# Kernel optimization log

Hardware: AMD Instinct MI355X
Metric: run time of the kernel (lower is better)

Reference implementation:

```python
import jax, jax.numpy as jnp
import numpy as np

SEQ_LEN = 168; PRED_LEN = 24; N_FEAT = 8; KERNEL = 25
N_QUBITS = 4; N_QLAYERS = 2; CONTEXT = 32; HIDDEN = 8; BATCH = 16384
LAG_POSITIONS = [1, 2, 3, 4, 5, 6, 23, 24, 25, 167, 168]
LAG_IDX = np.array([SEQ_LEN - l for l in LAG_POSITIONS if l <= SEQ_LEN])
N_LAGS = int(LAG_IDX.size)
PI = float(np.pi)


def _apply_1q(state, U, w):
    # apply 2x2 gate U (shared (2,2) or per-sample (B,2,2)) on wire w
    state = jnp.moveaxis(state, 1 + w, -1)
    if U.ndim == 2:
        state = jnp.einsum('ij,b...j->b...i', U, state)
    else:
        state = jnp.einsum('bij,b...j->b...i', U, state)
    return jnp.moveaxis(state, -1, 1 + w)


def _apply_cnot(state, c, t):
    ax_c, ax_t = 1 + c, 1 + t
    s0 = jax.lax.index_in_dim(state, 0, ax_c, keepdims=False)
    s1 = jax.lax.index_in_dim(state, 1, ax_c, keepdims=False)
    s1 = jnp.flip(s1, axis=ax_t - (1 if t > c else 0))
    return jnp.stack([s0, s1], axis=ax_c)


def _ry(theta):  # (B,) -> (B,2,2)
    c, s = jnp.cos(theta / 2), jnp.sin(theta / 2)
    return jnp.stack([jnp.stack([c, -s], -1), jnp.stack([s, c], -1)], -2).astype(jnp.complex64)


def _rot(w):  # w (3,): Rot(phi,theta,omega) = RZ(omega) RY(theta) RZ(phi)
    phi, theta, omega = w[0], w[1], w[2]
    c, s = jnp.cos(theta / 2), jnp.sin(theta / 2)
    ep = jnp.exp(-0.5j * (phi + omega))
    em = jnp.exp(0.5j * (phi - omega))
    return jnp.stack([jnp.stack([ep * c, -em * s]),
                      jnp.stack([jnp.conj(em) * s, jnp.conj(ep) * c])]).astype(jnp.complex64)


def _vqc(inputs, weights):
    # data re-uploading: [RY AngleEmbedding -> Rot per wire -> CNOT ring (range 1)] x N_QLAYERS
    # (StronglyEntanglingLayers is called with 1 layer per upload, so range is always 1)
    B = inputs.shape[0]
    state = jnp.zeros((B,) + (2,) * N_QUBITS, jnp.complex64)
    state = state.at[(slice(None),) + (0,) * N_QUBITS].set(1.0)
    for l in range(N_QLAYERS):
        for q in range(N_QUBITS):
            state = _apply_1q(state, _ry(inputs[:, q]), q)
        for q in range(N_QUBITS):
            state = _apply_1q(state, _rot(weights[l, q]), q)
        for q in range(N_QUBITS):
            state = _apply_cnot(state, q, (q + 1) % N_QUBITS)
    probs = state.real ** 2 + state.imag ** 2  # (B,2,2,2,2)
    zdiag = jnp.array([1.0, -1.0], jnp.float32)
    exps = []
    for q in range(N_QUBITS):
        other = tuple(a for a in range(1, N_QUBITS + 1) if a != 1 + q)
        exps.append(jnp.einsum('bq,q->b', probs.sum(other), zdiag))
    return jnp.stack(exps, axis=-1)  # (B, N_QUBITS)


def _decomp(x, decomp_w):
    # learnable moving-average decomposition (DLinear-style, per-feature softmax kernel, edge padding)
    pad = (KERNEL - 1) // 2
    w = jax.nn.softmax(decomp_w, axis=-1)  # (F,K)
    xp = jnp.pad(x, ((0, 0), (pad, KERNEL - 1 - pad), (0, 0)), mode='edge')
    xc = jnp.moveaxis(xp, 1, 2)  # (B,F,S+K-1)
    trend = jax.lax.conv_general_dilated(xc, w[:, None, :], (1,), 'VALID',
                                         feature_group_count=N_FEAT,
                                         dimension_numbers=('NCH', 'OIH', 'NCH'))
    trend = jnp.moveaxis(trend, 1, 2)  # (B,S,F)
    return x - trend, trend


def forward(x, decomp_w, trend_w, trend_b, seasonal_w, seasonal_b, h0_w, h0_b,
            ta_w, ta_b, sc_w, sc_b, crz_w, crz_b, cn_w, cn_b,
            vqc_r, vqc_u, vqc_c, expand_w, expand_b, mod_w, mod_b, fusion_alpha):
    seasonal, trend = _decomp(x, decomp_w)
    trend_out = jnp.einsum('bsf,ps->bpf', trend, trend_w) + trend_b[None, :, None]
    seasonal_base = jnp.einsum('bsf,ps->bpf', seasonal, seasonal_w) + seasonal_b[None, :, None]
    lag_vals = x[:, LAG_IDX, -1]  # (B, N_LAGS), demand is last feature
    h0 = jnp.tanh(lag_vals @ h0_w.T + h0_b)  # (B,H)
    ctx = jnp.einsum('bsf,cs->bfc', seasonal, ta_w) + ta_b  # (B,F,C)
    gru_in = jnp.tanh(ctx.reshape(x.shape[0], -1) @ sc_w.T + sc_b)  # (B,H)
    # single-step quantum GRU
    xh = jnp.concatenate([gru_in, h0], axis=1)  # (B,2H)
    rz_in = jnp.tanh(xh @ crz_w.T + crz_b) * PI  # r_in == z_in (same compress in source)
    r = jax.nn.sigmoid(_vqc(rz_in, vqc_r) @ expand_w.T + expand_b)
    z = jax.nn.sigmoid(_vqc(rz_in, vqc_u) @ expand_w.T + expand_b)
    n_in = jnp.tanh(jnp.concatenate([r * h0, gru_in], axis=1) @ cn_w.T + cn_b) * PI
    n = jnp.tanh(_vqc(n_in, vqc_c) @ expand_w.T + expand_b)
    h_new = (1 - z) * n + z * h0
    modulation = jnp.tanh(h_new @ mod_w.T + mod_b)  # (B,P)
    seasonal_out = seasonal_base * (1.0 + modulation[:, :, None])
    alpha = jax.nn.sigmoid(fusion_alpha)[0]
    return alpha * seasonal_out + (1 - alpha) * trend_out  # (B,P,F)


def setup_inputs() -> dict:
    key = jax.random.key(0)
    ks = iter(jax.random.split(key, 32))

    def lin(out_d, in_d):
        lim = 1.0 / np.sqrt(in_d)
        return (jax.random.uniform(next(ks), (out_d, in_d), jnp.float32, -lim, lim),
                jax.random.uniform(next(ks), (out_d,), jnp.float32, -lim, lim))

    trend_w, trend_b = lin(PRED_LEN, SEQ_LEN)
    seasonal_w, seasonal_b = lin(PRED_LEN, SEQ_LEN)
    h0_w, h0_b = lin(HIDDEN, N_LAGS)
    ta_w, ta_b = lin(CONTEXT, SEQ_LEN)
    sc_w, sc_b = lin(HIDDEN, N_FEAT * CONTEXT)
    crz_w, crz_b = lin(N_QUBITS, 2 * HIDDEN)
    cn_w, cn_b = lin(N_QUBITS, 2 * HIDDEN)
    expand_w, expand_b = lin(HIDDEN, N_QUBITS)
    mod_w, mod_b = lin(PRED_LEN, HIDDEN)
    return {
        'x': jax.random.normal(next(ks), (BATCH, SEQ_LEN, N_FEAT), jnp.float32),
        'decomp_w': 0.02 * jax.random.normal(next(ks), (N_FEAT, KERNEL), jnp.float32),
        'trend_w': trend_w, 'trend_b': trend_b,
        'seasonal_w': seasonal_w, 'seasonal_b': seasonal_b,
        'h0_w': h0_w, 'h0_b': h0_b,
        'ta_w': ta_w, 'ta_b': ta_b,
        'sc_w': sc_w, 'sc_b': sc_b,
        'crz_w': crz_w, 'crz_b': crz_b,
        'cn_w': cn_w, 'cn_b': cn_b,
        'vqc_r': jax.random.uniform(next(ks), (N_QLAYERS, N_QUBITS, 3), jnp.float32, 0.0, 2 * PI),
        'vqc_u': jax.random.uniform(next(ks), (N_QLAYERS, N_QUBITS, 3), jnp.float32, 0.0, 2 * PI),
        'vqc_c': jax.random.uniform(next(ks), (N_QLAYERS, N_QUBITS, 3), jnp.float32, 0.0, 2 * PI),
        'expand_w': expand_w, 'expand_b': expand_b,
        'mod_w': mod_w, 'mod_b': mod_b,
        'fusion_alpha': jnp.array([0.5], jnp.float32),
    }


def reference(x, decomp_w, trend_w, trend_b, seasonal_w, seasonal_b, h0_w, h0_b,
              ta_w, ta_b, sc_w, sc_b, crz_w, crz_b, cn_w, cn_b,
              vqc_r, vqc_u, vqc_c, expand_w, expand_b, mod_w, mod_b, fusion_alpha):
    return forward(x, decomp_w, trend_w, trend_b, seasonal_w, seasonal_b, h0_w, h0_b,
                   ta_w, ta_b, sc_w, sc_b, crz_w, crz_b, cn_w, cn_b,
                   vqc_r, vqc_u, vqc_c, expand_w, expand_b, mod_w, mod_b, fusion_alpha)
```

## Files before the change

kernel.cpp:

```cpp
#include <hip/hip_runtime.h>
#include <hip/hip_bf16.h>
#include <cmath>

#define SEQ   168
#define NF    8
#define PRED  24
#define HID   8
#define KTOT  1344
#define NSCH  6
#define PI_F  3.14159265358979323846f

#define WS_ROTC     256
#define WS_CGIN     512
#define WS_WT       1024
#define WS_IMG_BYTE 524288

typedef __attribute__((ext_vector_type(8))) short bf16x8;
typedef __attribute__((ext_vector_type(4))) float f32x4;

__device__ __forceinline__ float frcp(float x)  { return __builtin_amdgcn_rcpf(x); }
__device__ __forceinline__ float ftanh(float x) {
    float xc = fminf(fmaxf(x, -15.f), 15.f);
    float e  = __expf(2.f * xc);
    return (e - 1.f) * frcp(e + 1.f);
}
__device__ __forceinline__ float sigm(float x) { return frcp(1.f + __expf(-x)); }
__device__ __forceinline__ unsigned short f2bf(float f) {
    __hip_bfloat16 h = __float2bfloat16(f);
    return __builtin_bit_cast(unsigned short, h);
}
__device__ __forceinline__ unsigned pack2(float a, float b) {
    return (unsigned)f2bf(a) | ((unsigned)f2bf(b) << 16);
}

__global__ void k_compose(const float* __restrict__ decomp_w,
                          const float* __restrict__ trend_w,
                          const float* __restrict__ seasonal_w,
                          const float* __restrict__ ta_w,
                          float* __restrict__ Wt) {
    __shared__ float dwsh[NF * 25];
    int t = threadIdx.x;
    if (t < NF) {
        const float* row = decomp_w + t * 25;
        float m = row[0];
        for (int k = 1; k < 25; ++k) m = fmaxf(m, row[k]);
        float e[25]; float sum = 0.f;
        for (int k = 0; k < 25; ++k) { e[k] = expf(row[k] - m); sum += e[k]; }
        float inv = 1.f / sum;
        for (int k = 0; k < 25; ++k) dwsh[t * 25 + k] = e[k] * inv;
    }
    __syncthreads();
    int n = blockIdx.x * 256 + t;
    if (n >= SEQ * 640) return;
    int sx  = n / 640;
    int col = n % 640;
    int j = col >> 3;
    int f = col & 7;
    const float* dwf = dwsh + f * 25;
    const float* wsel;
    int isTrend = 0;
    if (j < 24)      { wsel = trend_w    + j        * SEQ; isTrend = 1; }
    else if (j < 48) { wsel = seasonal_w + (j - 24) * SEQ; }
    else             { wsel = ta_w       + (j - 48) * SEQ; }
    float acc = 0.f;
    if (sx == 0) {
        for (int s = 0; s <= 12; ++s) {
            float cw = 0.f;
            for (int k = 0; k <= 12 - s; ++k) cw += dwf[k];
            acc = fmaf(cw, wsel[s], acc);
        }
    } else if (sx == 167) {
        for (int s = 155; s < 168; ++s) {
            float cw = 0.f;
            for (int k = 179 - s; k < 25; ++k) cw += dwf[k];
            acc = fmaf(cw, wsel[s], acc);
        }
    } else {
        int lo = sx - 12; if (lo < 0) lo = 0;
        int hi = sx + 12; if (hi > 167) hi = 167;
        for (int s = lo; s <= hi; ++s) acc = fmaf(dwf[sx - s + 12], wsel[s], acc);
    }
    Wt[sx * 640 + col] = isTrend ? acc : (wsel[sx] - acc);
}

__global__ void k_img(const float* __restrict__ Wt, const float* __restrict__ sc_w,
                      const float* __restrict__ h0_w,
                      const float* __restrict__ vr, const float* __restrict__ vu,
                      const float* __restrict__ vc,
                      const float* __restrict__ sc_b, const float* __restrict__ ta_b,
                      float* __restrict__ rotc, float* __restrict__ cgin,
                      unsigned char* __restrict__ imgb) {
    int idx = blockIdx.x * 256 + threadIdx.x;
    if (idx < 12288) {
        int lane = idx & 63;
        int rest = idx >> 6;
        int ks = rest % 6;
        int fc = rest / 6;
        int cf = fc & 3, f = fc >> 2;
        int lr = lane & 15, lg = lane >> 4;
        unsigned short vals[8];
        #pragma unroll
        for (int e = 0; e < 8; ++e) {
            int k = ks * 32 + lg * 8 + e;
            float val = 0.f;
            if (k < SEQ) {
                if (cf < 3) {
                    int col = cf * 16 + lr;
                    val = Wt[k * 640 + (col & 1) * 192 + (col >> 1) * 8 + f];
                } else if (lr < 8) {
                    float a = 0.f;
                    for (int cc = 0; cc < 32; ++cc)
                        a = fmaf(sc_w[lr * 256 + f * 32 + cc], Wt[k * 640 + 384 + cc * 8 + f], a);
                    val = a;
                } else if (f == 7) {
                    const int LIDX[11] = {167,166,165,164,163,162,145,144,143,1,0};
                    #pragma unroll
                    for (int i = 0; i < 11; ++i)
                        if (k == LIDX[i]) val = h0_w[(lr - 8) * 11 + i];
                }
            }
            vals[e] = f2bf(val);
        }
        uint4 o;
        o.x = (unsigned)vals[0] | ((unsigned)vals[1] << 16);
        o.y = (unsigned)vals[2] | ((unsigned)vals[3] << 16);
        o.z = (unsigned)vals[4] | ((unsigned)vals[5] << 16);
        o.w = (unsigned)vals[6] | ((unsigned)vals[7] << 16);
        *(uint4*)(imgb + (size_t)rest * 1024 + lane * 16) = o;
    } else if (blockIdx.x == 48) {
        int t = threadIdx.x;
        if (t >= 64 && t < 88) {
            int n = t - 64;
            int v = n / 8, rest = n % 8;
            const float* w = (v == 0 ? vr : (v == 1 ? vu : vc)) + rest * 3;
            float phi = w[0], th = w[1], om = w[2];
            float c = cosf(0.5f * th), s = sinf(0.5f * th);
            float ap = -0.5f * (phi + om);
            float am =  0.5f * (phi - om);
            float* o = rotc + n * 4;
            o[0] = cosf(ap) * c;
            o[1] = sinf(ap) * c;
            o[2] = cosf(am) * s;
            o[3] = sinf(am) * s;
        } else if (t >= 96 && t < 104) {
            int h = t - 96;
            float a = sc_b[h];
            for (int cc = 0; cc < 32; ++cc) {
                float s = 0.f;
                for (int f = 0; f < 8; ++f) s += sc_w[h * 256 + f * 32 + cc];
                a = fmaf(ta_b[cc], s, a);
            }
            cgin[h] = a;
        }
    }
}

__device__ __forceinline__ float shflg(float v, int grp, int idx) {
    return __shfl(v, grp + idx, 64);
}

__device__ void vqc_run(const float cq[4], const float sq[4],
                        const float* __restrict__ rc,
                        int l, int grp, float exps[4]) {
    float re = (l == 0) ? 1.f : 0.f;
    float im = 0.f;
    #pragma unroll
    for (int layer = 0; layer < 2; ++layer) {
        #pragma unroll
        for (int q = 0; q < 4; ++q) {
            int m = 1 << (3 - q);
            float pre = shflg(re, grp, l ^ m);
            float pim = shflg(im, grp, l ^ m);
            float sg = (l & m) ? sq[q] : -sq[q];
            re = cq[q] * re + sg * pre;
            im = cq[q] * im + sg * pim;
        }
        #pragma unroll
        for (int q = 0; q < 4; ++q) {
            int m = 1 << (3 - q);
            const float* g = rc + (layer * 4 + q) * 4;
            float A = g[0], B = g[1], C = g[2], D = g[3];
            float pre = shflg(re, grp, l ^ m);
            float pim = shflg(im, grp, l ^ m);
            float car, cai, cpr, cpi;
            if (l & m) { car = A; cai = -B; cpr =  C; cpi = -D; }
            else       { car = A; cai =  B; cpr = -C; cpi = -D; }
            float nre = car * re - cai * im + cpr * pre - cpi * pim;
            float nim = car * im + cai * re + cpr * pim + cpi * pre;
            re = nre; im = nim;
        }
        #pragma unroll
        for (int q = 0; q < 4; ++q) {
            int mc = 1 << (3 - q);
            int mt = 1 << (3 - ((q + 1) & 3));
            float pre = shflg(re, grp, l ^ mt);
            float pim = shflg(im, grp, l ^ mt);
            if (l & mc) { re = pre; im = pim; }
        }
    }
    float prob = re * re + im * im;
    float v0 = (l & 8) ? -prob : prob;
    float v1 = (l & 4) ? -prob : prob;
    float v2 = (l & 2) ? -prob : prob;
    float v3 = (l & 1) ? -prob : prob;
    #pragma unroll
    for (int m = 1; m < 16; m <<= 1) {
        v0 += __shfl_xor(v0, m, 64);
        v1 += __shfl_xor(v1, m, 64);
        v2 += __shfl_xor(v2, m, 64);
        v3 += __shfl_xor(v3, m, 64);
    }
    exps[0] = v0; exps[1] = v1; exps[2] = v2; exps[3] = v3;
}

__global__ __launch_bounds__(512, 3)
void k_fused(const float* __restrict__ x, const unsigned char* __restrict__ img,
             const float* __restrict__ rotc, const float* __restrict__ cgin,
             const float* __restrict__ h0_b,
             const float* __restrict__ crz_w, const float* __restrict__ crz_b,
             const float* __restrict__ cn_w, const float* __restrict__ cn_b,
             const float* __restrict__ expand_w, const float* __restrict__ expand_b,
             const float* __restrict__ mod_w, const float* __restrict__ mod_b,
             const float* __restrict__ trend_b, const float* __restrict__ seasonal_b,
             const float* __restrict__ fusion_alpha,
             float* __restrict__ out, int Btot)
{
    __shared__ unsigned char lds[32768];
    float* ghpart = (float*)lds;
    float* ghbuf  = (float*)(lds + 16384);
    float* modt   = (float*)(lds + 16384 + 2304);

    const int t    = threadIdx.x;
    const int b0   = blockIdx.x * 32;
    const int w    = t >> 6, lane = t & 63, lr = lane & 15, lg = lane >> 4;

    const int arow  = t >> 4;
    const int spair = t & 15;
    int gr = b0 + arow; if (gr >= Btot) gr = Btot - 1;
    const float* xrow = x + (size_t)gr * KTOT;
    const unsigned char* ib = img + (size_t)(w * 24) * 1024 + (size_t)lane * 16;

    float4 ra[4];
    #pragma unroll
    for (int u = 0; u < 4; ++u) ra[u] = *(const float4*)&xrow[spair * 16 + u * 4];

    f32x4 acc[3][2], accg[2];
    #pragma unroll
    for (int cf = 0; cf < 3; ++cf) {
        acc[cf][0] = (f32x4){0.f, 0.f, 0.f, 0.f};
        acc[cf][1] = (f32x4){0.f, 0.f, 0.f, 0.f};
    }
    accg[0] = (f32x4){0.f, 0.f, 0.f, 0.f};
    accg[1] = (f32x4){0.f, 0.f, 0.f, 0.f};

    const int wb   = (arow * 64 + spair * 4) ^ ((arow & 7) << 4);
    const int ar0  = (lr * 64 + lg * 16) ^ ((lr & 7) << 4);
    const int ar1  = ((lr + 16) * 64 + lg * 16) ^ ((lr & 7) << 4);

    #pragma unroll
    for (int kc = 0; kc < NSCH; ++kc) {
        const int bufo = (kc & 1) * 16384;
        {
            const float* rf = (const float*)ra;
            #pragma unroll
            for (int f = 0; f < 8; ++f)
                *(unsigned*)&lds[bufo + f * 2048 + wb] = pack2(rf[f], rf[8 + f]);
        }
        if (kc + 1 < NSCH) {
            int off = (kc + 1) * 256 + spair * 16;
            if (off > KTOT - 16) off = KTOT - 16;
            #pragma unroll
            for (int u = 0; u < 4; ++u) ra[u] = *(const float4*)&xrow[off + u * 4];
        }
        bf16x8 Br[4];
        #pragma unroll
        for (int cf = 0; cf < 4; ++cf) Br[cf] = *(const bf16x8*)&ib[(cf * 6 + kc) * 1024];
        __syncthreads();
        {
            bf16x8 a0 = *(const bf16x8*)&lds[bufo + w * 2048 + ar0];
            bf16x8 a1 = *(const bf16x8*)&lds[bufo + w * 2048 + ar1];
            #pragma unroll
            for (int cf = 0; cf < 3; ++cf) {
                acc[cf][0] = __builtin_amdgcn_mfma_f32_16x16x32_bf16(a0, Br[cf], acc[cf][0], 0, 0, 0);
                acc[cf][1] = __builtin_amdgcn_mfma_f32_16x16x32_bf16(a1, Br[cf], acc[cf][1], 0, 0, 0);
            }
            accg[0] = __builtin_amdgcn_mfma_f32_16x16x32_bf16(a0, Br[3], accg[0], 0, 0, 0);
            accg[1] = __builtin_amdgcn_mfma_f32_16x16x32_bf16(a1, Br[3], accg[1], 0, 0, 0);
        }
    }

    #pragma unroll
    for (int mf = 0; mf < 2; ++mf)
        #pragma unroll
        for (int reg = 0; reg < 4; ++reg)
            ghpart[(w * 32 + mf * 16 + lg * 4 + reg) * 16 + lr] = accg[mf][reg];
    __syncthreads();
    {
        int row = t >> 4, col = t & 15;
        float s = 0.f;
        #pragma unroll
        for (int f = 0; f < 8; ++f) s += ghpart[f * 512 + row * 16 + col];
        ghbuf[row * 17 + col] = s;
    }
    __syncthreads();

    {
        const int rl  = t >> 4;
        const int l   = t & 15;
        const int grp = lane & 48;
        float gin[HID], h0v[HID];
        #pragma unroll
        for (int h = 0; h < HID; ++h) {
            gin[h] = ftanh(ghbuf[rl * 17 + h]     + cgin[h]);
            h0v[h] = ftanh(ghbuf[rl * 17 + 8 + h] + h0_b[h]);
        }
        float rz[4];
        #pragma unroll
        for (int q = 0; q < 4; ++q) {
            float a = crz_b[q];
            #pragma unroll
            for (int k = 0; k < 8; ++k) a = fmaf(gin[k], crz_w[q * 16 + k], a);
            #pragma unroll
            for (int k = 0; k < 8; ++k) a = fmaf(h0v[k], crz_w[q * 16 + 8 + k], a);
            rz[q] = ftanh(a) * PI_F;
        }
        float cq[4], sq[4];
        #pragma unroll
        for (int q = 0; q < 4; ++q) { cq[q] = __cosf(0.5f * rz[q]); sq[q] = __sinf(0.5f * rz[q]); }

        float er[4], ez[4];
        vqc_run(cq, sq, rotc + 0 * 32, l, grp, er);
        vqc_run(cq, sq, rotc + 1 * 32, l, grp, ez);

        float rr[HID], zz[HID];
        #pragma unroll
        for (int h = 0; h < HID; ++h) {
            float a = expand_b[h], b = expand_b[h];
            #pragma unroll
            for (int q = 0; q < 4; ++q) {
                a = fmaf(er[q], expand_w[h * 4 + q], a);
                b = fmaf(ez[q], expand_w[h * 4 + q], b);
            }
            rr[h] = sigm(a);
            zz[h] = sigm(b);
        }
        float ni[4];
        #pragma unroll
        for (int q = 0; q < 4; ++q) {
            float a = cn_b[q];
            #pragma unroll
            for (int k = 0; k < 8; ++k) a = fmaf(rr[k] * h0v[k], cn_w[q * 16 + k], a);
            #pragma unroll
            for (int k = 0; k < 8; ++k) a = fmaf(gin[k], cn_w[q * 16 + 8 + k], a);
            ni[q] = ftanh(a) * PI_F;
        }
        #pragma unroll
        for (int q = 0; q < 4; ++q) { cq[q] = __cosf(0.5f * ni[q]); sq[q] = __sinf(0.5f * ni[q]); }
        float en[4];
        vqc_run(cq, sq, rotc + 2 * 32, l, grp, en);

        float hn[HID];
        #pragma unroll
        for (int h = 0; h < HID; ++h) {
            float a = expand_b[h];
            #pragma unroll
            for (int q = 0; q < 4; ++q) a = fmaf(en[q], expand_w[h * 4 + q], a);
            float nn = ftanh(a);
            hn[h] = (1.f - zz[h]) * nn + zz[h] * h0v[h];
        }
        int pp = l;
        float a = mod_b[pp];
        #pragma unroll
        for (int h = 0; h < HID; ++h) a = fmaf(hn[h], mod_w[pp * 8 + h], a);
        modt[rl * 25 + pp] = ftanh(a);
        if (l < 8) {
            pp = l + 16;
            a = mod_b[pp];
            #pragma unroll
            for (int h = 0; h < HID; ++h) a = fmaf(hn[h], mod_w[pp * 8 + h], a);
            modt[rl * 25 + pp] = ftanh(a);
        }
    }
    __syncthreads();

    const float alpha = sigm(fusion_alpha[0]);
    #pragma unroll
    for (int cf = 0; cf < 3; ++cf) {
        int p = cf * 8 + (lr >> 1);
        float tb = trend_b[p], sb = seasonal_b[p];
        #pragma unroll
        for (int mf = 0; mf < 2; ++mf) {
            #pragma unroll
            for (int reg = 0; reg < 4; ++reg) {
                int rl = mf * 16 + lg * 4 + reg;
                float v  = acc[cf][mf][reg];
                float pt = __shfl_xor(v, 1, 64);
                if (!(lr & 1)) {
                    int R = b0 + rl;
                    if (R < Btot) {
                        float md = modt[rl * 25 + p];
                        float res = alpha * ((pt + sb) * (1.f + md))
                                  + (1.f - alpha) * (v + tb);
                        out[(size_t)R * 192 + p * 8 + w] = res;
                    }
                }
            }
        }
    }
}

extern "C" void kernel_launch(void* const* d_in, const int* in_sizes, int n_in,
                              void* d_out, int out_size, void* d_ws, size_t ws_size,
                              hipStream_t stream) {
    const float* x          = (const float*)d_in[0];
    const float* decomp_w   = (const float*)d_in[1];
    const float* trend_w    = (const float*)d_in[2];
    const float* trend_b    = (const float*)d_in[3];
    const float* seasonal_w = (const float*)d_in[4];
    const float* seasonal_b = (const float*)d_in[5];
    const float* h0_w       = (const float*)d_in[6];
    const float* h0_b       = (const float*)d_in[7];
    const float* ta_w       = (const float*)d_in[8];
    const float* ta_b       = (const float*)d_in[9];
    const float* sc_w       = (const float*)d_in[10];
    const float* sc_b       = (const float*)d_in[11];
    const float* crz_w      = (const float*)d_in[12];
    const float* crz_b      = (const float*)d_in[13];
    const float* cn_w       = (const float*)d_in[14];
    const float* cn_b       = (const float*)d_in[15];
    const float* vqc_r      = (const float*)d_in[16];
    const float* vqc_u      = (const float*)d_in[17];
    const float* vqc_c      = (const float*)d_in[18];
    const float* expand_w   = (const float*)d_in[19];
    const float* expand_b   = (const float*)d_in[20];
    const float* mod_w      = (const float*)d_in[21];
    const float* mod_b      = (const float*)d_in[22];
    const float* fus_a      = (const float*)d_in[23];
    float* out = (float*)d_out;

    float* ws   = (float*)d_ws;
    float* rotc = ws + WS_ROTC;
    float* cgin = ws + WS_CGIN;
    float* Wt   = ws + WS_WT;
    unsigned char* img = (unsigned char*)d_ws + WS_IMG_BYTE;

    const int Btot = in_sizes[0] / (SEQ * NF);

    k_compose<<<(SEQ * 640 + 255) / 256, 256, 0, stream>>>(decomp_w, trend_w, seasonal_w, ta_w, Wt);
    k_img<<<49, 256, 0, stream>>>(Wt, sc_w, h0_w, vqc_r, vqc_u, vqc_c, sc_b, ta_b,
                                  rotc, cgin, img);

    k_fused<<<(Btot + 31) / 32, 512, 0, stream>>>(x, img, rotc, cgin, h0_b,
                                                  crz_w, crz_b, cn_w, cn_b,
                                                  expand_w, expand_b, mod_w, mod_b,
                                                  trend_b, seasonal_b, fus_a, out, Btot);
}
```

Before: 49.59 us.

## Halve rows per block to 16 and raise occupancy target

Each 512-thread block now processes 16 batch rows instead of 32. Each wave issues one 16-row MFMA tile per feature instead of two, the LDS footprint halves, and the launch bound asks for 8 blocks per CU instead of 3. The x loads are split across two thread halves, and the B-fragment loads are interleaved with the MFMAs. The aim is to raise occupancy and hide memory latency. In exchange the grid doubles, the B image is re-read twice as often per row, and half the threads sit idle in the quantum and modulation tail.

```diff
diff --git a/kernel.cpp b/kernel.cpp
--- a/kernel.cpp
+++ b/kernel.cpp
@@ -213,7 +213,7 @@
     exps[0] = v0; exps[1] = v1; exps[2] = v2; exps[3] = v3;
 }
 
-__global__ __launch_bounds__(512, 3)
+__global__ __launch_bounds__(512, 8)
 void k_fused(const float* __restrict__ x, const unsigned char* __restrict__ img,
              const float* __restrict__ rotc, const float* __restrict__ cgin,
              const float* __restrict__ h0_b,
@@ -225,89 +225,84 @@
              const float* __restrict__ fusion_alpha,
              float* __restrict__ out, int Btot)
 {
-    __shared__ unsigned char lds[32768];
+    __shared__ unsigned char lds[16384];
     float* ghpart = (float*)lds;
-    float* ghbuf  = (float*)(lds + 16384);
-    float* modt   = (float*)(lds + 16384 + 2304);
+    float* ghbuf  = (float*)(lds + 8192);
+    float* modt   = (float*)(lds + 8192 + 1152);
 
     const int t    = threadIdx.x;
-    const int b0   = blockIdx.x * 32;
+    const int b0   = blockIdx.x * 16;
     const int w    = t >> 6, lane = t & 63, lr = lane & 15, lg = lane >> 4;
 
-    const int arow  = t >> 4;
+    const int arow  = t >> 5;
     const int spair = t & 15;
+    const int fh    = (t >> 4) & 1;
     int gr = b0 + arow; if (gr >= Btot) gr = Btot - 1;
     const float* xrow = x + (size_t)gr * KTOT;
     const unsigned char* ib = img + (size_t)(w * 24) * 1024 + (size_t)lane * 16;
 
-    float4 ra[4];
-    #pragma unroll
-    for (int u = 0; u < 4; ++u) ra[u] = *(const float4*)&xrow[spair * 16 + u * 4];
-
-    f32x4 acc[3][2], accg[2];
-    #pragma unroll
-    for (int cf = 0; cf < 3; ++cf) {
-        acc[cf][0] = (f32x4){0.f, 0.f, 0.f, 0.f};
-        acc[cf][1] = (f32x4){0.f, 0.f, 0.f, 0.f};
-    }
-    accg[0] = (f32x4){0.f, 0.f, 0.f, 0.f};
-    accg[1] = (f32x4){0.f, 0.f, 0.f, 0.f};
-
-    const int wb   = (arow * 64 + spair * 4) ^ ((arow & 7) << 4);
-    const int ar0  = (lr * 64 + lg * 16) ^ ((lr & 7) << 4);
-    const int ar1  = ((lr + 16) * 64 + lg * 16) ^ ((lr & 7) << 4);
+    float4 ra0, ra1;
+    {
+        int o0 = spair * 16 + fh * 4;
+        ra0 = *(const float4*)&xrow[o0];
+        ra1 = *(const float4*)&xrow[o0 + 8];
+    }
+
+    f32x4 acc[3], accg;
+    #pragma unroll
+    for (int cf = 0; cf < 3; ++cf) acc[cf] = (f32x4){0.f, 0.f, 0.f, 0.f};
+    accg = (f32x4){0.f, 0.f, 0.f, 0.f};
+
+    const int wb  = (arow * 64 + spair * 4) ^ ((arow & 7) << 4);
+    const int ard = (lr * 64 + lg * 16) ^ ((lr & 7) << 4);
 
     #pragma unroll
     for (int kc = 0; kc < NSCH; ++kc) {
-        const int bufo = (kc & 1) * 16384;
+        const int bufo = (kc & 1) * 8192;
         {
-            const float* rf = (const float*)ra;
-            #pragma unroll
-            for (int f = 0; f < 8; ++f)
-                *(unsigned*)&lds[bufo + f * 2048 + wb] = pack2(rf[f], rf[8 + f]);
+            const float* r0 = (const float*)&ra0;
+            const float* r1 = (const float*)&ra1;
+            #pragma unroll
+            for (int f = 0; f < 4; ++f)
+                *(unsigned*)&lds[bufo + (fh * 4 + f) * 1024 + wb] = pack2(r0[f], r1[f]);
         }
         if (kc + 1 < NSCH) {
-            int off = (kc + 1) * 256 + spair * 16;
-            if (off > KTOT - 16) off = KTOT - 16;
-            #pragma unroll
-            for (int u = 0; u < 4; ++u) ra[u] = *(const float4*)&xrow[off + u * 4];
-        }
-        bf16x8 Br[4];
-        #pragma unroll
-        for (int cf = 0; cf < 4; ++cf) Br[cf] = *(const bf16x8*)&ib[(cf * 6 + kc) * 1024];
+            int o0 = (kc + 1) * 256 + spair * 16 + fh * 4;
+            int o1 = o0 + 8;
+            if (o0 > KTOT - 4) o0 = KTOT - 4;
+            if (o1 > KTOT - 4) o1 = KTOT - 4;
+            ra0 = *(const float4*)&xrow[o0];
+            ra1 = *(const float4*)&xrow[o1];
+        }
+        bf16x8 Br0 = *(const bf16x8*)&ib[(0 * 6 + kc) * 1024];
+        bf16x8 Br1 = *(const bf16x8*)&ib[(1 * 6 + kc) * 1024];
         __syncthreads();
-        {
-            bf16x8 a0 = *(const bf16x8*)&lds[bufo + w * 2048 + ar0];
-            bf16x8 a1 = *(const bf16x8*)&lds[bufo + w * 2048 + ar1];
-            #pragma unroll
-            for (int cf = 0; cf < 3; ++cf) {
-                acc[cf][0] = __builtin_amdgcn_mfma_f32_16x16x32_bf16(a0, Br[cf], acc[cf][0], 0, 0, 0);
-                acc[cf][1] = __builtin_amdgcn_mfma_f32_16x16x32_bf16(a1, Br[cf], acc[cf][1], 0, 0, 0);
-            }
-            accg[0] = __builtin_amdgcn_mfma_f32_16x16x32_bf16(a0, Br[3], accg[0], 0, 0, 0);
-            accg[1] = __builtin_amdgcn_mfma_f32_16x16x32_bf16(a1, Br[3], accg[1], 0, 0, 0);
-        }
-    }
-
-    #pragma unroll
-    for (int mf = 0; mf < 2; ++mf)
-        #pragma unroll
-        for (int reg = 0; reg < 4; ++reg)
-            ghpart[(w * 32 + mf * 16 + lg * 4 + reg) * 16 + lr] = accg[mf][reg];
+        bf16x8 a0 = *(const bf16x8*)&lds[bufo + w * 1024 + ard];
+        acc[0] = __builtin_amdgcn_mfma_f32_16x16x32_bf16(a0, Br0, acc[0], 0, 0, 0);
+        acc[1] = __builtin_amdgcn_mfma_f32_16x16x32_bf16(a0, Br1, acc[1], 0, 0, 0);
+        bf16x8 Br2 = *(const bf16x8*)&ib[(2 * 6 + kc) * 1024];
+        bf16x8 Br3 = *(const bf16x8*)&ib[(3 * 6 + kc) * 1024];
+        acc[2] = __builtin_amdgcn_mfma_f32_16x16x32_bf16(a0, Br2, acc[2], 0, 0, 0);
+        accg   = __builtin_amdgcn_mfma_f32_16x16x32_bf16(a0, Br3, accg,   0, 0, 0);
+    }
+
+    #pragma unroll
+    for (int reg = 0; reg < 4; ++reg)
+        ghpart[w * 256 + (lg * 4 + reg) * 16 + lr] = accg[reg];
     __syncthreads();
-    {
+    if (t < 256) {
         int row = t >> 4, col = t & 15;
         float s = 0.f;
         #pragma unroll
-        for (int f = 0; f < 8; ++f) s += ghpart[f * 512 + row * 16 + col];
+        for (int f = 0; f < 8; ++f) s += ghpart[f * 256 + row * 16 + col];
         ghbuf[row * 17 + col] = s;
     }
     __syncthreads();
 
-    {
+    if (t < 256) {
         const int rl  = t >> 4;
         const int l   = t & 15;
-        const int grp = lane & 48;
+        const int grp = (t & 63) & 48;
         float gin[HID], h0v[HID];
         #pragma unroll
         for (int h = 0; h < HID; ++h) {
@@ -389,20 +384,17 @@
         int p = cf * 8 + (lr >> 1);
         float tb = trend_b[p], sb = seasonal_b[p];
         #pragma unroll
-        for (int mf = 0; mf < 2; ++mf) {
-            #pragma unroll
-            for (int reg = 0; reg < 4; ++reg) {
-                int rl = mf * 16 + lg * 4 + reg;
-                float v  = acc[cf][mf][reg];
-                float pt = __shfl_xor(v, 1, 64);
-                if (!(lr & 1)) {
-                    int R = b0 + rl;
-                    if (R < Btot) {
-                        float md = modt[rl * 25 + p];
-                        float res = alpha * ((pt + sb) * (1.f + md))
-                                  + (1.f - alpha) * (v + tb);
-                        out[(size_t)R * 192 + p * 8 + w] = res;
-                    }
+        for (int reg = 0; reg < 4; ++reg) {
+            int rl = lg * 4 + reg;
+            float v  = acc[cf][reg];
+            float pt = __shfl_xor(v, 1, 64);
+            if (!(lr & 1)) {
+                int R = b0 + rl;
+                if (R < Btot) {
+                    float md = modt[rl * 25 + p];
+                    float res = alpha * ((pt + sb) * (1.f + md))
+                              + (1.f - alpha) * (v + tb);
+                    out[(size_t)R * 192 + p * 8 + w] = res;
                 }
             }
         }
@@ -450,7 +442,7 @@
     k_img<<<49, 256, 0, stream>>>(Wt, sc_w, h0_w, vqc_r, vqc_u, vqc_c, sc_b, ta_b,
                                   rotc, cgin, img);
 
-    k_fused<<<(Btot + 31) / 32, 512, 0, stream>>>(x, img, rotc, cgin, h0_b,
+    k_fused<<<(Btot + 15) / 16, 512, 0, stream>>>(x, img, rotc, cgin, h0_b,
                                                   crz_w, crz_b, cn_w, cn_b,
                                                   expand_w, expand_b, mod_w, mod_b,
                                                   trend_b, seasonal_b, fus_a, out, Btot);
```

After: 58.41 us. 1.18x slower.
